# Kernel tuning notes

Measured on AMD Instinct MI355X. Metric: run time of the kernel, lower is better.

The kernel has to match this reference:

```python
import jax, jax.numpy as jnp
import numpy as np

EPS = 1e-5

def _bn_relu(h, gamma, beta):
    # h: (b, c, n); BatchNorm1d in training mode: stats over (batch, spatial)
    mean = jnp.mean(h, axis=(0, 2), keepdims=True)
    var = jnp.var(h, axis=(0, 2), keepdims=True)
    h = (h - mean) * jax.lax.rsqrt(var + EPS)
    h = h * gamma[None, :, None] + beta[None, :, None]
    return jax.nn.relu(h)

def setup_inputs() -> dict:
    key = jax.random.key(0)
    ks = jax.random.split(key, 8)
    b, c, n, k, N = 4, 128, 4096, 32, 16384
    x = jax.random.normal(ks[0], (b, c, n, k), dtype=jnp.float32)
    group_idx = jax.random.randint(ks[1], (b, n, k), 0, N, dtype=jnp.int64)
    fps_idx = jax.random.randint(ks[2], (b, n), 0, N, dtype=jnp.int64)
    w1 = jax.random.normal(ks[3], (c, 2 * c), dtype=jnp.float32) * (1.0 / np.sqrt(2 * c))
    b1 = jnp.zeros((c,), dtype=jnp.float32)
    g1 = jnp.ones((c,), dtype=jnp.float32)
    be1 = jnp.zeros((c,), dtype=jnp.float32)
    w2 = jax.random.normal(ks[4], (c, c), dtype=jnp.float32) * (1.0 / np.sqrt(c))
    b2 = jnp.zeros((c,), dtype=jnp.float32)
    g2 = jnp.ones((c,), dtype=jnp.float32)
    be2 = jnp.zeros((c,), dtype=jnp.float32)
    return {"x": x, "group_idx": group_idx, "fps_idx": fps_idx, "N": N,
            "w1": w1, "b1": b1, "g1": g1, "be1": be1,
            "w2": w2, "b2": b2, "g2": g2, "be2": be2}

def reference(x, group_idx, fps_idx, N, w1, b1, g1, be1, w2, b2, g2, be2):
    b, c, n, k = x.shape
    # local max pool over neighbors: (b, c, n)
    group_x = jnp.max(x, axis=-1)
    # scatter_max of (b, n*k, c) into (b, N, c), out initialized to zeros
    dil = jnp.transpose(x, (0, 2, 3, 1)).reshape(b * n * k, c)
    idx = group_idx.reshape(b, n * k) + (jnp.arange(b, dtype=group_idx.dtype) * N)[:, None]
    seg = jax.ops.segment_max(dil, idx.reshape(-1), num_segments=b * N)
    # torch scatter_max with zero-initialized out: max with 0, empty segs -> 0
    seg = jnp.maximum(seg, 0.0).reshape(b, N, c)
    # gather FPS-sampled points: (b, n, c) -> (b, c, n)
    gathered = jnp.take_along_axis(seg, fps_idx[:, :, None], axis=1)
    dilated_x = jnp.transpose(gathered, (0, 2, 1))
    feat = jnp.concatenate([group_x, dilated_x], axis=1)  # (b, 2c, n)
    h = jnp.einsum('oc,bcn->bon', w1, feat) + b1[None, :, None]
    h = _bn_relu(h, g1, be1)
    h = jnp.einsum('oc,bcn->bon', w2, h) + b2[None, :, None]
    h = _bn_relu(h, g2, be2)
    return h
```

## Files before the change

kernel.cpp:

```cpp
#include <hip/hip_runtime.h>

constexpr int Bb = 4, Cc = 128, Nn = 4096, Kk = 32, Ns = 16384;
constexpr int ROWS = Bb * Nn;
constexpr int NK = Nn * Kk;
constexpr float EPS = 1e-5f;

typedef __attribute__((ext_vector_type(8))) short short8;
typedef __attribute__((ext_vector_type(4))) float f32x4;

__device__ __forceinline__ unsigned short f2bf(float f) {
    unsigned int u = __float_as_uint(f);
    unsigned int r = u + 0x7FFFu + ((u >> 16) & 1u);
    return (unsigned short)(r >> 16);
}

constexpr size_t SZ_SEG   = (size_t)Bb * Ns * Cc * 4;
constexpr size_t OFF_SEG  = 0;
constexpr size_t SZ_GX    = (size_t)ROWS * Cc * 4;
constexpr size_t OFF_GX   = OFF_SEG + SZ_SEG;
constexpr size_t OFF_H1   = OFF_GX + SZ_GX;
constexpr size_t OFF_H2   = OFF_H1 + SZ_GX;
constexpr size_t SZ_PART  = (size_t)256 * 128 * 2 * 4;
constexpr size_t OFF_P1   = OFF_H2 + SZ_GX;
constexpr size_t OFF_P2   = OFF_P1 + SZ_PART;
constexpr size_t OFF_FLAG = OFF_P2 + SZ_PART;

__global__ __launch_bounds__(256) void k_prep(const int* __restrict__ fps,
                                              float4* __restrict__ seg4,
                                              int* __restrict__ flags) {
    int i = blockIdx.x * 8 + (threadIdx.x >> 5);
    int lane = threadIdx.x & 31;
    int bb = i >> 12;
    int fi = fps[i];
    if (lane == 0) flags[bb * Ns + fi] = i;
    seg4[((size_t)bb * Ns + fi) * 32 + lane] = float4{0.f, 0.f, 0.f, 0.f};
}

__global__ __launch_bounds__(256) void k_scatter(
        const float* __restrict__ x, const int* __restrict__ gidx,
        const int* __restrict__ flags, const int* __restrict__ fps,
        float* __restrict__ gx, unsigned int* __restrict__ seg) {
    int nn = blockIdx.x, bb = blockIdx.y;
    int t = threadIdx.x;
    __shared__ float tile[128][33];
    __shared__ float gbuf[128];
    __shared__ unsigned int srow[32];
    __shared__ int klist[32];
    __shared__ int nflag;

    if (t == 0) nflag = 0;
    __syncthreads();
    if (t < 32) {
        int idxv = gidx[((bb * Nn + nn) << 5) + t];
        srow[t] = (unsigned int)(bb * Ns + idxv) * 128u;
        int fl = flags[bb * Ns + idxv];
        int j = fl & 16383;
        if (((j >> 12) == bb) && (fps[j] == idxv)) {
            int pos = atomicAdd(&nflag, 1);
            klist[pos] = t;
        }
    }

    int k4 = (t & 7) * 4;
    int cq = t >> 3;
    const float* xb = x + (size_t)bb * Cc * NK + (size_t)nn * Kk;
    float4 v[4];
    #pragma unroll
    for (int p = 0; p < 4; p++)
        v[p] = *(const float4*)(xb + (size_t)(cq + p * 32) * NK + k4);

    #pragma unroll
    for (int p = 0; p < 4; p++) {
        int ch = cq + p * 32;
        float4 w = v[p];
        float m = fmaxf(fmaxf(w.x, w.y), fmaxf(w.z, w.w));
        m = fmaxf(m, __shfl_xor(m, 1, 64));
        m = fmaxf(m, __shfl_xor(m, 2, 64));
        m = fmaxf(m, __shfl_xor(m, 4, 64));
        if ((t & 7) == 0) gbuf[ch] = m;
        tile[ch][k4 + 0] = w.x; tile[ch][k4 + 1] = w.y;
        tile[ch][k4 + 2] = w.z; tile[ch][k4 + 3] = w.w;
    }
    __syncthreads();

    int nf = nflag;
    int ch = t & 127, rep = t >> 7;
    for (int it = rep; it < nf; it += 2) {
        int k = klist[it];
        float val = tile[ch][k];
        if (val > 0.f) atomicMax(seg + srow[k] + ch, __float_as_uint(val));
    }
    if (t < 128) gx[((size_t)(bb * Nn + nn)) * 128 + t] = gbuf[t];
}

__global__ __launch_bounds__(512) void k_gemm1(
        const float* __restrict__ gx, const float* __restrict__ segf,
        const int* __restrict__ fps, const float* __restrict__ w1,
        const float* __restrict__ b1, float* __restrict__ h1,
        float* __restrict__ part) {
    __shared__ __align__(16) unsigned short A_lds[64][72];
    __shared__ __align__(16) unsigned short B_lds[128][72];
    __shared__ float reds[4][128], redq[4][128];
    __shared__ int rowbase[64];
    int t = threadIdx.x;
    int m0 = blockIdx.x * 64;
    if (t < 64) rowbase[t] = (((m0 + t) >> 12) * Ns + fps[m0 + t]) * 128;
    int w = t >> 6, l = t & 63;
    int r0 = (w >> 1) * 16, c0 = (w & 1) * 64;
    int lr = l & 15, lk = (l >> 4) * 8;
    f32x4 acc[4] = {};
    for (int k0 = 0; k0 < 256; k0 += 64) {
        __syncthreads();
        #pragma unroll
        for (int i = 0; i < 2; i++) {
            int q = t + i * 512;
            int row = q >> 4, kq = (q & 15) * 4;
            int k = k0 + kq;
            float4 v;
            if (k0 < 128) v = *(const float4*)(gx + (size_t)(m0 + row) * 128 + k);
            else          v = *(const float4*)(segf + rowbase[row] + (k - 128));
            ushort4 o{f2bf(v.x), f2bf(v.y), f2bf(v.z), f2bf(v.w)};
            *(ushort4*)&A_lds[row][kq] = o;
        }
        #pragma unroll
        for (int i = 0; i < 4; i++) {
            int q = t + i * 512;
            int col = q >> 4, kq = (q & 15) * 4;
            float4 v = *(const float4*)(w1 + (size_t)col * 256 + k0 + kq);
            ushort4 o{f2bf(v.x), f2bf(v.y), f2bf(v.z), f2bf(v.w)};
            *(ushort4*)&B_lds[col][kq] = o;
        }
        __syncthreads();
        #pragma unroll
        for (int ks = 0; ks < 2; ks++) {
            short8 a = *(const short8*)&A_lds[r0 + lr][ks * 32 + lk];
            #pragma unroll
            for (int cb = 0; cb < 4; cb++) {
                short8 b = *(const short8*)&B_lds[c0 + cb * 16 + lr][ks * 32 + lk];
                acc[cb] = __builtin_amdgcn_mfma_f32_16x16x32_bf16(a, b, acc[cb], 0, 0, 0);
            }
        }
    }
    int orow = m0 + r0 + (l >> 4) * 4;
    #pragma unroll
    for (int cb = 0; cb < 4; cb++) {
        int col = c0 + cb * 16 + lr;
        float bias = b1[col];
        float sv = 0.f, qv = 0.f;
        #pragma unroll
        for (int r = 0; r < 4; r++) {
            float o = acc[cb][r] + bias;
            h1[(size_t)(orow + r) * 128 + col] = o;
            sv += o; qv += o * o;
        }
        sv += __shfl_xor(sv, 16, 64); sv += __shfl_xor(sv, 32, 64);
        qv += __shfl_xor(qv, 16, 64); qv += __shfl_xor(qv, 32, 64);
        if (l < 16) { reds[w >> 1][col] = sv; redq[w >> 1][col] = qv; }
    }
    __syncthreads();
    if (t < 128) {
        float s = reds[0][t] + reds[1][t] + reds[2][t] + reds[3][t];
        float q = redq[0][t] + redq[1][t] + redq[2][t] + redq[3][t];
        part[blockIdx.x * 128 + t] = s;
        part[32768 + blockIdx.x * 128 + t] = q;
    }
}

__global__ __launch_bounds__(512) void k_gemm2(
        const float* __restrict__ h1, const float* __restrict__ part1,
        const float* __restrict__ g1, const float* __restrict__ be1,
        const float* __restrict__ w2, const float* __restrict__ b2,
        float* __restrict__ h2, float* __restrict__ part2) {
    __shared__ __align__(16) unsigned short A_lds[64][72];
    __shared__ __align__(16) unsigned short B_lds[128][72];
    __shared__ float reds[4][128], redq[4][128];
    __shared__ float ssc[128], ssh[128], tmp[256];
    int t = threadIdx.x;
    int m0 = blockIdx.x * 64;
    if (t < 256) {
        int ch = t & 127;
        const float* src = part1 + (t >> 7) * 32768 + ch;
        float a = 0.f;
        #pragma unroll 8
        for (int j = 0; j < 256; j++) a += src[j * 128];
        tmp[t] = a;
    }
    __syncthreads();
    if (t < 128) {
        float mean = tmp[t] * (1.0f / 16384.0f);
        float var = tmp[t + 128] * (1.0f / 16384.0f) - mean * mean;
        float sc = g1[t] * rsqrtf(var + EPS);
        ssc[t] = sc;
        ssh[t] = be1[t] - mean * sc;
    }
    __syncthreads();
    int w = t >> 6, l = t & 63;
    int r0 = (w >> 1) * 16, c0 = (w & 1) * 64;
    int lr = l & 15, lk = (l >> 4) * 8;
    f32x4 acc[4] = {};
    for (int k0 = 0; k0 < 128; k0 += 64) {
        __syncthreads();
        #pragma unroll
        for (int i = 0; i < 2; i++) {
            int q = t + i * 512;
            int row = q >> 4, kq = (q & 15) * 4;
            int k = k0 + kq;
            float4 v = *(const float4*)(h1 + (size_t)(m0 + row) * 128 + k);
            float a0 = fmaxf(0.f, fmaf(v.x, ssc[k + 0], ssh[k + 0]));
            float a1 = fmaxf(0.f, fmaf(v.y, ssc[k + 1], ssh[k + 1]));
            float a2 = fmaxf(0.f, fmaf(v.z, ssc[k + 2], ssh[k + 2]));
            float a3 = fmaxf(0.f, fmaf(v.w, ssc[k + 3], ssh[k + 3]));
            ushort4 o{f2bf(a0), f2bf(a1), f2bf(a2), f2bf(a3)};
            *(ushort4*)&A_lds[row][kq] = o;
        }
        #pragma unroll
        for (int i = 0; i < 4; i++) {
            int q = t + i * 512;
            int col = q >> 4, kq = (q & 15) * 4;
            float4 v = *(const float4*)(w2 + (size_t)col * 128 + k0 + kq);
            ushort4 o{f2bf(v.x), f2bf(v.y), f2bf(v.z), f2bf(v.w)};
            *(ushort4*)&B_lds[col][kq] = o;
        }
        __syncthreads();
        #pragma unroll
        for (int ks = 0; ks < 2; ks++) {
            short8 a = *(const short8*)&A_lds[r0 + lr][ks * 32 + lk];
            #pragma unroll
            for (int cb = 0; cb < 4; cb++) {
                short8 b = *(const short8*)&B_lds[c0 + cb * 16 + lr][ks * 32 + lk];
                acc[cb] = __builtin_amdgcn_mfma_f32_16x16x32_bf16(a, b, acc[cb], 0, 0, 0);
            }
        }
    }
    int orow = m0 + r0 + (l >> 4) * 4;
    #pragma unroll
    for (int cb = 0; cb < 4; cb++) {
        int col = c0 + cb * 16 + lr;
        float bias = b2[col];
        float sv = 0.f, qv = 0.f;
        #pragma unroll
        for (int r = 0; r < 4; r++) {
            float o = acc[cb][r] + bias;
            h2[(size_t)(orow + r) * 128 + col] = o;
            sv += o; qv += o * o;
        }
        sv += __shfl_xor(sv, 16, 64); sv += __shfl_xor(sv, 32, 64);
        qv += __shfl_xor(qv, 16, 64); qv += __shfl_xor(qv, 32, 64);
        if (l < 16) { reds[w >> 1][col] = sv; redq[w >> 1][col] = qv; }
    }
    __syncthreads();
    if (t < 128) {
        float s = reds[0][t] + reds[1][t] + reds[2][t] + reds[3][t];
        float q = redq[0][t] + redq[1][t] + redq[2][t] + redq[3][t];
        part2[blockIdx.x * 128 + t] = s;
        part2[32768 + blockIdx.x * 128 + t] = q;
    }
}

__global__ __launch_bounds__(512) void k_out(const float* __restrict__ h2,
                                             const float* __restrict__ part2,
                                             const float* __restrict__ g2,
                                             const float* __restrict__ be2,
                                             float* __restrict__ out) {
    __shared__ float tile[64][129];
    __shared__ float lsc[128], lsh[128], tmp[256];
    int t = threadIdx.x;
    int bb = blockIdx.y, n0 = blockIdx.x * 64;
    if (t < 256) {
        int ch = t & 127;
        const float* src = part2 + (t >> 7) * 32768 + ch;
        float a = 0.f;
        #pragma unroll 8
        for (int j = 0; j < 256; j++) a += src[j * 128];
        tmp[t] = a;
    }
    __syncthreads();
    if (t < 128) {
        float mean = tmp[t] * (1.0f / 16384.0f);
        float var = tmp[t + 128] * (1.0f / 16384.0f) - mean * mean;
        float sc = g2[t] * rsqrtf(var + EPS);
        lsc[t] = sc;
        lsh[t] = be2[t] - mean * sc;
    }
    #pragma unroll
    for (int i = 0; i < 4; i++) {
        int fq = t + i * 512;
        int row = fq >> 5;
        int c4 = (fq & 31) * 4;
        float4 v = *(const float4*)(h2 + ((size_t)(bb * Nn + n0 + row)) * 128 + c4);
        tile[row][c4 + 0] = v.x; tile[row][c4 + 1] = v.y;
        tile[row][c4 + 2] = v.z; tile[row][c4 + 3] = v.w;
    }
    __syncthreads();
    int j = t & 63, og = t >> 6;
    #pragma unroll
    for (int o = og; o < 128; o += 8) {
        float v = fmaxf(0.f, fmaf(tile[j][o], lsc[o], lsh[o]));
        out[((size_t)(bb * 128 + o)) * Nn + n0 + j] = v;
    }
}

extern "C" void kernel_launch(void* const* d_in, const int* in_sizes, int n_in,
                              void* d_out, int out_size, void* d_ws, size_t ws_size,
                              hipStream_t stream) {
    const float* x    = (const float*)d_in[0];
    const int*   gidx = (const int*)d_in[1];
    const int*   fps  = (const int*)d_in[2];
    const float* w1   = (const float*)d_in[4];
    const float* b1   = (const float*)d_in[5];
    const float* g1   = (const float*)d_in[6];
    const float* be1  = (const float*)d_in[7];
    const float* w2   = (const float*)d_in[8];
    const float* b2   = (const float*)d_in[9];
    const float* g2   = (const float*)d_in[10];
    const float* be2  = (const float*)d_in[11];
    float* out = (float*)d_out;

    char* ws = (char*)d_ws;
    unsigned int* seg  = (unsigned int*)(ws + OFF_SEG);
    float* segf        = (float*)(ws + OFF_SEG);
    float4* seg4       = (float4*)(ws + OFF_SEG);
    float* gx          = (float*)(ws + OFF_GX);
    float* h1          = (float*)(ws + OFF_H1);
    float* h2          = (float*)(ws + OFF_H2);
    float* part1       = (float*)(ws + OFF_P1);
    float* part2       = (float*)(ws + OFF_P2);
    int* flags         = (int*)(ws + OFF_FLAG);

    k_prep<<<ROWS / 8, 256, 0, stream>>>(fps, seg4, flags);
    k_scatter<<<dim3(Nn, Bb), 256, 0, stream>>>(x, gidx, flags, fps, gx, seg);
    k_gemm1<<<ROWS / 64, 512, 0, stream>>>(gx, segf, fps, w1, b1, h1, part1);
    k_gemm2<<<ROWS / 64, 512, 0, stream>>>(h1, part1, g1, be1, w2, b2, h2, part2);
    k_out<<<dim3(Nn / 64, Bb), 512, 0, stream>>>(h2, part2, g2, be2, out);
}
```

Before: 124.9 us.

## Halve GEMM tiles, hoist BN stat finalize into tiny kernels, bitmask scatter

```diff
diff --git a/kernel.cpp b/kernel.cpp
--- a/kernel.cpp
+++ b/kernel.cpp
@@ -3,6 +3,8 @@
 constexpr int Bb = 4, Cc = 128, Nn = 4096, Kk = 32, Ns = 16384;
 constexpr int ROWS = Bb * Nn;
 constexpr int NK = Nn * Kk;
+constexpr int NPART = 512;
+constexpr int QOFF = NPART * 128;
 constexpr float EPS = 1e-5f;
 
 typedef __attribute__((ext_vector_type(8))) short short8;
@@ -20,10 +22,14 @@
 constexpr size_t OFF_GX   = OFF_SEG + SZ_SEG;
 constexpr size_t OFF_H1   = OFF_GX + SZ_GX;
 constexpr size_t OFF_H2   = OFF_H1 + SZ_GX;
-constexpr size_t SZ_PART  = (size_t)256 * 128 * 2 * 4;
+constexpr size_t SZ_PART  = (size_t)NPART * 128 * 2 * 4;
 constexpr size_t OFF_P1   = OFF_H2 + SZ_GX;
 constexpr size_t OFF_P2   = OFF_P1 + SZ_PART;
 constexpr size_t OFF_FLAG = OFF_P2 + SZ_PART;
+constexpr size_t OFF_SC1  = OFF_FLAG + (size_t)Bb * Ns * 4;
+constexpr size_t OFF_SH1  = OFF_SC1 + 512;
+constexpr size_t OFF_SC2  = OFF_SH1 + 512;
+constexpr size_t OFF_SH2  = OFF_SC2 + 512;
 
 __global__ __launch_bounds__(256) void k_prep(const int* __restrict__ fps,
                                               float4* __restrict__ seg4,
@@ -45,29 +51,31 @@
     __shared__ float tile[128][33];
     __shared__ float gbuf[128];
     __shared__ unsigned int srow[32];
-    __shared__ int klist[32];
-    __shared__ int nflag;
-
-    if (t == 0) nflag = 0;
-    __syncthreads();
+    __shared__ unsigned int fmask;
+
+    if (t == 0) fmask = 0u;
+    __syncthreads();
+
+    int k4 = (t & 7) * 4;
+    int cq = t >> 3;
+    const float* xb = x + (size_t)bb * Cc * NK + (size_t)nn * Kk;
+    float4 v[4];
+    #pragma unroll
+    for (int p = 0; p < 4; p++)
+        v[p] = *(const float4*)(xb + (size_t)(cq + p * 32) * NK + k4);
+
     if (t < 32) {
         int idxv = gidx[((bb * Nn + nn) << 5) + t];
         srow[t] = (unsigned int)(bb * Ns + idxv) * 128u;
         int fl = flags[bb * Ns + idxv];
         int j = fl & 16383;
-        if (((j >> 12) == bb) && (fps[j] == idxv)) {
-            int pos = atomicAdd(&nflag, 1);
-            klist[pos] = t;
-        }
-    }
-
-    int k4 = (t & 7) * 4;
-    int cq = t >> 3;
-    const float* xb = x + (size_t)bb * Cc * NK + (size_t)nn * Kk;
-    float4 v[4];
-    #pragma unroll
-    for (int p = 0; p < 4; p++)
-        v[p] = *(const float4*)(xb + (size_t)(cq + p * 32) * NK + k4);
+        if (((j >> 12) == bb) && (fps[j] == idxv)) atomicOr(&fmask, 1u << t);
+    }
+    __syncthreads();
+
+    unsigned int mask = fmask;
+    bool f0 = (mask >> (k4 + 0)) & 1, f1 = (mask >> (k4 + 1)) & 1;
+    bool f2 = (mask >> (k4 + 2)) & 1, f3 = (mask >> (k4 + 3)) & 1;
 
     #pragma unroll
     for (int p = 0; p < 4; p++) {
@@ -78,19 +86,25 @@
         m = fmaxf(m, __shfl_xor(m, 2, 64));
         m = fmaxf(m, __shfl_xor(m, 4, 64));
         if ((t & 7) == 0) gbuf[ch] = m;
-        tile[ch][k4 + 0] = w.x; tile[ch][k4 + 1] = w.y;
-        tile[ch][k4 + 2] = w.z; tile[ch][k4 + 3] = w.w;
-    }
-    __syncthreads();
-
-    int nf = nflag;
+        if (f0) tile[ch][k4 + 0] = w.x;
+        if (f1) tile[ch][k4 + 1] = w.y;
+        if (f2) tile[ch][k4 + 2] = w.z;
+        if (f3) tile[ch][k4 + 3] = w.w;
+    }
+    __syncthreads();
+
+    if (t < 128) gx[((size_t)(bb * Nn + nn)) * 128 + t] = gbuf[t];
+
     int ch = t & 127, rep = t >> 7;
-    for (int it = rep; it < nf; it += 2) {
-        int k = klist[it];
+    unsigned int m = mask;
+    if (rep && m) m &= m - 1;
+    while (m) {
+        int k = __ffs(m) - 1;
         float val = tile[ch][k];
         if (val > 0.f) atomicMax(seg + srow[k] + ch, __float_as_uint(val));
-    }
-    if (t < 128) gx[((size_t)(bb * Nn + nn)) * 128 + t] = gbuf[t];
+        m &= m - 1;
+        if (m) m &= m - 1;
+    }
 }
 
 __global__ __launch_bounds__(512) void k_gemm1(
@@ -98,23 +112,21 @@
         const int* __restrict__ fps, const float* __restrict__ w1,
         const float* __restrict__ b1, float* __restrict__ h1,
         float* __restrict__ part) {
-    __shared__ __align__(16) unsigned short A_lds[64][72];
+    __shared__ __align__(16) unsigned short A_lds[32][72];
     __shared__ __align__(16) unsigned short B_lds[128][72];
-    __shared__ float reds[4][128], redq[4][128];
-    __shared__ int rowbase[64];
-    int t = threadIdx.x;
-    int m0 = blockIdx.x * 64;
-    if (t < 64) rowbase[t] = (((m0 + t) >> 12) * Ns + fps[m0 + t]) * 128;
+    __shared__ float reds[8][32], redq[8][32];
+    __shared__ int rowbase[32];
+    int t = threadIdx.x;
+    int m0 = blockIdx.x * 32;
+    if (t < 32) rowbase[t] = (((m0 + t) >> 12) * Ns + fps[m0 + t]) * 128;
     int w = t >> 6, l = t & 63;
-    int r0 = (w >> 1) * 16, c0 = (w & 1) * 64;
+    int r0 = (w >> 2) * 16, c0 = (w & 3) * 32;
     int lr = l & 15, lk = (l >> 4) * 8;
-    f32x4 acc[4] = {};
+    f32x4 acc[2] = {};
     for (int k0 = 0; k0 < 256; k0 += 64) {
         __syncthreads();
-        #pragma unroll
-        for (int i = 0; i < 2; i++) {
-            int q = t + i * 512;
-            int row = q >> 4, kq = (q & 15) * 4;
+        {
+            int row = t >> 4, kq = (t & 15) * 4;
             int k = k0 + kq;
             float4 v;
             if (k0 < 128) v = *(const float4*)(gx + (size_t)(m0 + row) * 128 + k);
@@ -135,7 +147,7 @@
         for (int ks = 0; ks < 2; ks++) {
             short8 a = *(const short8*)&A_lds[r0 + lr][ks * 32 + lk];
             #pragma unroll
-            for (int cb = 0; cb < 4; cb++) {
+            for (int cb = 0; cb < 2; cb++) {
                 short8 b = *(const short8*)&B_lds[c0 + cb * 16 + lr][ks * 32 + lk];
                 acc[cb] = __builtin_amdgcn_mfma_f32_16x16x32_bf16(a, b, acc[cb], 0, 0, 0);
             }
@@ -143,7 +155,7 @@
     }
     int orow = m0 + r0 + (l >> 4) * 4;
     #pragma unroll
-    for (int cb = 0; cb < 4; cb++) {
+    for (int cb = 0; cb < 2; cb++) {
         int col = c0 + cb * 16 + lr;
         float bias = b1[col];
         float sv = 0.f, qv = 0.f;
@@ -155,55 +167,59 @@
         }
         sv += __shfl_xor(sv, 16, 64); sv += __shfl_xor(sv, 32, 64);
         qv += __shfl_xor(qv, 16, 64); qv += __shfl_xor(qv, 32, 64);
-        if (l < 16) { reds[w >> 1][col] = sv; redq[w >> 1][col] = qv; }
+        if (l < 16) { reds[w][cb * 16 + l] = sv; redq[w][cb * 16 + l] = qv; }
     }
     __syncthreads();
     if (t < 128) {
-        float s = reds[0][t] + reds[1][t] + reds[2][t] + reds[3][t];
-        float q = redq[0][t] + redq[1][t] + redq[2][t] + redq[3][t];
-        part[blockIdx.x * 128 + t] = s;
-        part[32768 + blockIdx.x * 128 + t] = q;
-    }
-}
-
-__global__ __launch_bounds__(512) void k_gemm2(
-        const float* __restrict__ h1, const float* __restrict__ part1,
-        const float* __restrict__ g1, const float* __restrict__ be1,
-        const float* __restrict__ w2, const float* __restrict__ b2,
-        float* __restrict__ h2, float* __restrict__ part2) {
-    __shared__ __align__(16) unsigned short A_lds[64][72];
-    __shared__ __align__(16) unsigned short B_lds[128][72];
-    __shared__ float reds[4][128], redq[4][128];
-    __shared__ float ssc[128], ssh[128], tmp[256];
-    int t = threadIdx.x;
-    int m0 = blockIdx.x * 64;
-    if (t < 256) {
-        int ch = t & 127;
-        const float* src = part1 + (t >> 7) * 32768 + ch;
-        float a = 0.f;
-        #pragma unroll 8
-        for (int j = 0; j < 256; j++) a += src[j * 128];
-        tmp[t] = a;
-    }
+        int g = t >> 5, o = t & 31;
+        part[blockIdx.x * 128 + t] = reds[g][o] + reds[g + 4][o];
+        part[QOFF + blockIdx.x * 128 + t] = redq[g][o] + redq[g + 4][o];
+    }
+}
+
+__global__ __launch_bounds__(256) void k_fin(const float* __restrict__ part,
+                                             const float* __restrict__ g,
+                                             const float* __restrict__ be,
+                                             float* __restrict__ scale,
+                                             float* __restrict__ shift) {
+    __shared__ float tmp[256];
+    int t = threadIdx.x;
+    int ch = t & 127;
+    const float* src = part + (t >> 7) * QOFF + ch;
+    float a = 0.f;
+    #pragma unroll 8
+    for (int j = 0; j < NPART; j++) a += src[j * 128];
+    tmp[t] = a;
     __syncthreads();
     if (t < 128) {
         float mean = tmp[t] * (1.0f / 16384.0f);
         float var = tmp[t + 128] * (1.0f / 16384.0f) - mean * mean;
-        float sc = g1[t] * rsqrtf(var + EPS);
-        ssc[t] = sc;
-        ssh[t] = be1[t] - mean * sc;
-    }
-    __syncthreads();
+        float sc = g[t] * rsqrtf(var + EPS);
+        scale[t] = sc;
+        shift[t] = be[t] - mean * sc;
+    }
+}
+
+__global__ __launch_bounds__(512) void k_gemm2(
+        const float* __restrict__ h1, const float* __restrict__ sc1,
+        const float* __restrict__ sh1, const float* __restrict__ w2,
+        const float* __restrict__ b2, float* __restrict__ h2,
+        float* __restrict__ part2) {
+    __shared__ __align__(16) unsigned short A_lds[32][72];
+    __shared__ __align__(16) unsigned short B_lds[128][72];
+    __shared__ float reds[8][32], redq[8][32];
+    __shared__ float ssc[128], ssh[128];
+    int t = threadIdx.x;
+    int m0 = blockIdx.x * 32;
+    if (t < 128) { ssc[t] = sc1[t]; ssh[t] = sh1[t]; }
     int w = t >> 6, l = t & 63;
-    int r0 = (w >> 1) * 16, c0 = (w & 1) * 64;
+    int r0 = (w >> 2) * 16, c0 = (w & 3) * 32;
     int lr = l & 15, lk = (l >> 4) * 8;
-    f32x4 acc[4] = {};
+    f32x4 acc[2] = {};
     for (int k0 = 0; k0 < 128; k0 += 64) {
         __syncthreads();
-        #pragma unroll
-        for (int i = 0; i < 2; i++) {
-            int q = t + i * 512;
-            int row = q >> 4, kq = (q & 15) * 4;
+        {
+            int row = t >> 4, kq = (t & 15) * 4;
             int k = k0 + kq;
             float4 v = *(const float4*)(h1 + (size_t)(m0 + row) * 128 + k);
             float a0 = fmaxf(0.f, fmaf(v.x, ssc[k + 0], ssh[k + 0]));
@@ -226,7 +242,7 @@
         for (int ks = 0; ks < 2; ks++) {
             short8 a = *(const short8*)&A_lds[r0 + lr][ks * 32 + lk];
             #pragma unroll
-            for (int cb = 0; cb < 4; cb++) {
+            for (int cb = 0; cb < 2; cb++) {
                 short8 b = *(const short8*)&B_lds[c0 + cb * 16 + lr][ks * 32 + lk];
                 acc[cb] = __builtin_amdgcn_mfma_f32_16x16x32_bf16(a, b, acc[cb], 0, 0, 0);
             }
@@ -234,7 +250,7 @@
     }
     int orow = m0 + r0 + (l >> 4) * 4;
     #pragma unroll
-    for (int cb = 0; cb < 4; cb++) {
+    for (int cb = 0; cb < 2; cb++) {
         int col = c0 + cb * 16 + lr;
         float bias = b2[col];
         float sv = 0.f, qv = 0.f;
@@ -246,44 +262,27 @@
         }
         sv += __shfl_xor(sv, 16, 64); sv += __shfl_xor(sv, 32, 64);
         qv += __shfl_xor(qv, 16, 64); qv += __shfl_xor(qv, 32, 64);
-        if (l < 16) { reds[w >> 1][col] = sv; redq[w >> 1][col] = qv; }
+        if (l < 16) { reds[w][cb * 16 + l] = sv; redq[w][cb * 16 + l] = qv; }
     }
     __syncthreads();
     if (t < 128) {
-        float s = reds[0][t] + reds[1][t] + reds[2][t] + reds[3][t];
-        float q = redq[0][t] + redq[1][t] + redq[2][t] + redq[3][t];
-        part2[blockIdx.x * 128 + t] = s;
-        part2[32768 + blockIdx.x * 128 + t] = q;
+        int g = t >> 5, o = t & 31;
+        part2[blockIdx.x * 128 + t] = reds[g][o] + reds[g + 4][o];
+        part2[QOFF + blockIdx.x * 128 + t] = redq[g][o] + redq[g + 4][o];
     }
 }
 
 __global__ __launch_bounds__(512) void k_out(const float* __restrict__ h2,
-                                             const float* __restrict__ part2,
-                                             const float* __restrict__ g2,
-                                             const float* __restrict__ be2,
+                                             const float* __restrict__ sc2,
+                                             const float* __restrict__ sh2,
                                              float* __restrict__ out) {
-    __shared__ float tile[64][129];
-    __shared__ float lsc[128], lsh[128], tmp[256];
-    int t = threadIdx.x;
-    int bb = blockIdx.y, n0 = blockIdx.x * 64;
-    if (t < 256) {
-        int ch = t & 127;
-        const float* src = part2 + (t >> 7) * 32768 + ch;
-        float a = 0.f;
-        #pragma unroll 8
-        for (int j = 0; j < 256; j++) a += src[j * 128];
-        tmp[t] = a;
-    }
-    __syncthreads();
-    if (t < 128) {
-        float mean = tmp[t] * (1.0f / 16384.0f);
-        float var = tmp[t + 128] * (1.0f / 16384.0f) - mean * mean;
-        float sc = g2[t] * rsqrtf(var + EPS);
-        lsc[t] = sc;
-        lsh[t] = be2[t] - mean * sc;
-    }
-    #pragma unroll
-    for (int i = 0; i < 4; i++) {
+    __shared__ float tile[32][129];
+    __shared__ float lsc[128], lsh[128];
+    int t = threadIdx.x;
+    int bb = blockIdx.y, n0 = blockIdx.x * 32;
+    if (t < 128) { lsc[t] = sc2[t]; lsh[t] = sh2[t]; }
+    #pragma unroll
+    for (int i = 0; i < 2; i++) {
         int fq = t + i * 512;
         int row = fq >> 5;
         int c4 = (fq & 31) * 4;
@@ -292,9 +291,9 @@
         tile[row][c4 + 2] = v.z; tile[row][c4 + 3] = v.w;
     }
     __syncthreads();
-    int j = t & 63, og = t >> 6;
-    #pragma unroll
-    for (int o = og; o < 128; o += 8) {
+    int j = t & 31, og = t >> 5;
+    #pragma unroll
+    for (int o = og; o < 128; o += 16) {
         float v = fmaxf(0.f, fmaf(tile[j][o], lsc[o], lsh[o]));
         out[((size_t)(bb * 128 + o)) * Nn + n0 + j] = v;
     }
@@ -326,10 +325,16 @@
     float* part1       = (float*)(ws + OFF_P1);
     float* part2       = (float*)(ws + OFF_P2);
     int* flags         = (int*)(ws + OFF_FLAG);
+    float* sc1         = (float*)(ws + OFF_SC1);
+    float* sh1         = (float*)(ws + OFF_SH1);
+    float* sc2         = (float*)(ws + OFF_SC2);
+    float* sh2         = (float*)(ws + OFF_SH2);
 
     k_prep<<<ROWS / 8, 256, 0, stream>>>(fps, seg4, flags);
     k_scatter<<<dim3(Nn, Bb), 256, 0, stream>>>(x, gidx, flags, fps, gx, seg);
-    k_gemm1<<<ROWS / 64, 512, 0, stream>>>(gx, segf, fps, w1, b1, h1, part1);
-    k_gemm2<<<ROWS / 64, 512, 0, stream>>>(h1, part1, g1, be1, w2, b2, h2, part2);
-    k_out<<<dim3(Nn / 64, Bb), 512, 0, stream>>>(h2, part2, g2, be2, out);
-}
+    k_gemm1<<<ROWS / 32, 512, 0, stream>>>(gx, segf, fps, w1, b1, h1, part1);
+    k_fin<<<1, 256, 0, stream>>>(part1, g1, be1, sc1, sh1);
+    k_gemm2<<<ROWS / 32, 512, 0, stream>>>(h1, sc1, sh1, w2, b2, h2, part2);
+    k_fin<<<1, 256, 0, stream>>>(part2, g2, be2, sc2, sh2);
+    k_out<<<dim3(Nn / 32, Bb), 512, 0, stream>>>(h2, sc2, sh2, out);
+}
```

Result: slower. 141.6 us (+13.4%).
